# Kernel tuning notes

Hardware: AMD Instinct MI355X
Metric: run time of the kernel (lower is better)

## Reference

```python
import jax, jax.numpy as jnp
import numpy as np

B, N, C = 8, 4096, 512
H = 8
HD = C // H          # head_dim = 64
KS = 5               # dwc kernel size
FF = 3.0             # focusing factor


def setup_inputs() -> dict:
    key = jax.random.key(0)
    ks = jax.random.split(key, 8)
    s = 1.0 / np.sqrt(C)
    return {
        "x": jax.random.normal(ks[0], (B, N, C), dtype=jnp.float32),
        "Wq": jax.random.normal(ks[1], (C, C), dtype=jnp.float32) * s,
        "Wkv": jax.random.normal(ks[2], (C, 2 * C), dtype=jnp.float32) * s,
        "Wproj": jax.random.normal(ks[3], (C, C), dtype=jnp.float32) * s,
        "b_proj": jax.random.normal(ks[4], (C,), dtype=jnp.float32) * 0.01,
        "scale_param": jnp.zeros((1, 1, C), dtype=jnp.float32),  # nn.Parameter(zeros)
        "dwc_w": jax.random.normal(ks[5], (HD, 1, KS, KS), dtype=jnp.float32) * 0.1,
        "dwc_b": jax.random.normal(ks[6], (HD,), dtype=jnp.float32) * 0.01,
    }


def _focus(t):
    # power-focusing map: preserve L2 norm while sharpening via elementwise power
    n = jnp.linalg.norm(t, axis=-1, keepdims=True)
    tp = t ** FF
    return tp / jnp.linalg.norm(tp, axis=-1, keepdims=True) * n


def reference(x, Wq, Wkv, Wproj, b_proj, scale_param, dwc_w, dwc_b):
    b, n, cdim = x.shape
    q = jax.nn.relu(x @ Wq) + 1e-6                      # [B,N,C]
    kv = x @ Wkv
    k = jax.nn.relu(kv[..., :cdim]) + 1e-6              # [B,N,C]
    v = kv[..., cdim:]                                  # [B,N,C]
    scale = jax.nn.softplus(scale_param)
    q = _focus(q / scale)
    k = _focus(k / scale)

    def split_heads(t):  # b n (h c) -> (b h) n c
        return t.reshape(b, n, H, HD).transpose(0, 2, 1, 3).reshape(b * H, n, HD)

    q, k, v = split_heads(q), split_heads(k), split_heads(v)
    i = j = n; c = d = HD
    z = 1.0 / (jnp.einsum('bic,bc->bi', q, k.sum(axis=1)) + 1e-6)  # [(bh), n]
    if i * j * (c + d) > c * d * (i + j):
        # linear path: O(N*c*d)
        kvm = jnp.einsum('bjc,bjd->bcd', k, v)          # [(bh), c, d]
        out = jnp.einsum('bic,bcd,bi->bid', q, kvm, z)
    else:
        qk = jnp.einsum('bic,bjc->bij', q, k)
        out = jnp.einsum('bij,bjd,bi->bid', qk, v, z)

    num = int(n ** 0.5)  # 64; N must be a perfect square
    fm = q.reshape(b * H, num, num, HD).transpose(0, 3, 1, 2)  # b c w h
    fm = jax.lax.conv_general_dilated(
        fm, dwc_w, window_strides=(1, 1), padding='SAME',
        feature_group_count=HD,
        dimension_numbers=('NCHW', 'OIHW', 'NCHW')) + dwc_b[None, :, None, None]
    fm = fm.transpose(0, 2, 3, 1).reshape(b * H, n, HD)
    out = out + fm
    out = out.reshape(b, H, n, HD).transpose(0, 2, 1, 3).reshape(b, n, cdim)
    return out @ Wproj + b_proj
```

## Files before the change

kernel.cpp:

```cpp
#include <hip/hip_runtime.h>
#include <cstddef>
#include <cstdint>

#define B_ 8
#define N_ 4096
#define C_ 512
#define H_ 8
#define HD_ 64
#define BH_ 64

typedef short  bf16x8 __attribute__((ext_vector_type(8)));
typedef float  f32x4  __attribute__((ext_vector_type(4)));
typedef ushort u16x8  __attribute__((ext_vector_type(8)));
typedef ushort u16x4  __attribute__((ext_vector_type(4)));

__device__ __forceinline__ float softplusf(float p) {
  return (p > 20.f) ? p : log1pf(expf(p));
}

__device__ __forceinline__ ushort f2bf(float f) {
  union { float f; unsigned u; } c; c.f = f;
  const unsigned r = c.u + 0x7fffu + ((c.u >> 16) & 1u);
  return (ushort)(r >> 16);
}
__device__ __forceinline__ float bf2f(ushort h) {
  union { unsigned u; float f; } c; c.u = ((unsigned)h) << 16;
  return c.f;
}

#define GLOAD16(g, l)                                                        \
  __builtin_amdgcn_global_load_lds(                                          \
      (const __attribute__((address_space(1))) void*)(g),                    \
      (__attribute__((address_space(3))) void*)(l), 16, 0, 0)

__global__ void scale_kernel(const float* __restrict__ sp, float* __restrict__ sinv)
{
  const int c = threadIdx.x;
  sinv[c] = 1.f / softplusf(sp[c]);
}

__global__ __launch_bounds__(256) void cvt_hi(const float* __restrict__ in,
                                              ushort* __restrict__ hi)
{
  const size_t i = (size_t)blockIdx.x * 256 + threadIdx.x;
  const float4 a = ((const float4*)in)[i * 2];
  const float4 b = ((const float4*)in)[i * 2 + 1];
  const float f[8] = {a.x, a.y, a.z, a.w, b.x, b.y, b.z, b.w};
  u16x8 h;
  #pragma unroll
  for (int j = 0; j < 8; ++j) h[j] = f2bf(f[j]);
  *(u16x8*)&hi[i * 8] = h;
}

__global__ __launch_bounds__(256) void cvt_w_t(const float* __restrict__ in,
                                               ushort* __restrict__ hi, int Nn)
{
  const int t  = blockIdx.x * 256 + threadIdx.x;
  const int n  = t >> 6;
  const int k8 = (t & 63) * 8;
  u16x8 h;
  #pragma unroll
  for (int j = 0; j < 8; ++j) h[j] = f2bf(in[(size_t)(k8 + j) * Nn + n]);
  *(u16x8*)&hi[(size_t)n * 512 + k8] = h;
}

__global__ __launch_bounds__(512, 2) void gemm_bf16(
    const ushort* __restrict__ Ah, const ushort* __restrict__ Bh,
    const float* __restrict__ bias,
    ushort* __restrict__ ob0, ushort* __restrict__ ob1, ushort* __restrict__ ob2,
    float* __restrict__ outf,
    int ncolb, int s1, int s2, int r0, int r1, int r2)
{
  __shared__ ushort lds[2][32768];
  const int tid = threadIdx.x;
  const int bid = blockIdx.x;
  const int loc = bid >> 3;
  const int xcd = bid & 7;
  const int row0 = ((xcd << 4) + loc / ncolb) * 256;
  const int col0 = (loc % ncolb) * 256;

  const int lane = tid & 63;
  const int li   = lane & 15;
  const int kq   = lane >> 4;
  const int w    = tid >> 6;
  const int wr   = (w >> 2) * 128;
  const int wc   = (w & 3) * 64;
  const int wbase = tid & 448;

  f32x4 acc[8][4] = {};

  auto STAGE = [&](int buf, int t) {
    ushort* l = &lds[buf][0];
    const int k0 = t * 64;
    #pragma unroll
    for (int it = 0; it < 4; ++it) {
      const int c   = it * 512 + tid;
      const int cw  = it * 512 + wbase;
      const int kb  = c >> 8;
      const int row = c & 255;
      GLOAD16(Ah + (size_t)(row0 + row) * 512 + k0 + kb * 8, &l[cw * 8]);
    }
    #pragma unroll
    for (int it = 0; it < 4; ++it) {
      const int c   = it * 512 + tid;
      const int cw  = it * 512 + wbase;
      const int kb  = c >> 8;
      const int col = c & 255;
      GLOAD16(Bh + (size_t)(col0 + col) * 512 + k0 + kb * 8, &l[16384 + cw * 8]);
    }
  };

  auto COMPUTE = [&](int buf) {
    const ushort* l = &lds[buf][0];
    #pragma unroll
    for (int kk = 0; kk < 2; ++kk) {
      const int kb = kk * 4 + kq;
      bf16x8 bv[4];
      #pragma unroll
      for (int n = 0; n < 4; ++n)
        bv[n] = *(const bf16x8*)&l[16384 + (kb * 256 + wc + n * 16 + li) * 8];
      __builtin_amdgcn_s_setprio(1);
      #pragma unroll
      for (int m = 0; m < 8; ++m) {
        const bf16x8 av = *(const bf16x8*)&l[(kb * 256 + wr + m * 16 + li) * 8];
        #pragma unroll
        for (int n = 0; n < 4; ++n)
          acc[m][n] = __builtin_amdgcn_mfma_f32_16x16x32_bf16(av, bv[n], acc[m][n], 0, 0, 0);
      }
      __builtin_amdgcn_s_setprio(0);
    }
  };

  STAGE(0, 0);
  __syncthreads();
  #pragma unroll 1
  for (int t = 0; t < 3; ++t) {
    STAGE(1, 2 * t + 1);
    COMPUTE(0);
    __syncthreads();
    STAGE(0, 2 * t + 2);
    COMPUTE(1);
    __syncthreads();
  }
  STAGE(1, 7);
  COMPUTE(0);
  __syncthreads();
  COMPUTE(1);

  if (outf) {
    #pragma unroll
    for (int m = 0; m < 8; ++m)
      #pragma unroll
      for (int n = 0; n < 4; ++n) {
        const int col = col0 + wc + n * 16 + li;
        const int row = row0 + wr + m * 16 + kq * 4;
        const float bv = bias[col];
        #pragma unroll
        for (int r = 0; r < 4; ++r)
          outf[(size_t)(row + r) * 512 + col] = acc[m][n][r] + bv;
      }
  } else {
    ushort* dest; int cbase, relu;
    if (col0 < s1)      { dest = ob0; cbase = 0;  relu = r0; }
    else if (col0 < s2) { dest = ob1; cbase = s1; relu = r1; }
    else                { dest = ob2; cbase = s2; relu = r2; }
    #pragma unroll
    for (int m = 0; m < 8; ++m)
      #pragma unroll
      for (int n = 0; n < 4; ++n) {
        const int col = col0 + wc + n * 16 + li;
        const int row = row0 + wr + m * 16 + kq * 4;
        #pragma unroll
        for (int r = 0; r < 4; ++r) {
          float v = acc[m][n][r];
          if (relu) v = fmaxf(v, 0.f) + 1e-6f;
          dest[(size_t)(row + r) * 512 + (col - cbase)] = f2bf(v);
        }
      }
  }
}

__global__ __launch_bounds__(256) void focus2(ushort* __restrict__ qb, ushort* __restrict__ kb,
                                              const float* __restrict__ sinv)
{
  const int rid  = blockIdx.x * 4 + (threadIdx.x >> 6);
  const int lane = threadIdx.x & 63;
  ushort* t = (rid < B_ * N_) ? qb : kb;
  const int row = rid & (B_ * N_ - 1);
  ushort* p = t + (size_t)row * 512 + lane * 8;
  const u16x8 raw = *(const u16x8*)p;
  const float4 sa = *(const float4*)&sinv[lane * 8];
  const float4 sb = *(const float4*)&sinv[lane * 8 + 4];
  const float sc[8] = {sa.x, sa.y, sa.z, sa.w, sb.x, sb.y, sb.z, sb.w};
  float tv[8];
  float s2 = 0.f, s6 = 0.f;
  #pragma unroll
  for (int i = 0; i < 8; ++i) {
    const float x = bf2f(raw[i]) * sc[i];
    tv[i] = x;
    const float x3 = x * x * x;
    s2 = fmaf(x, x, s2);
    s6 = fmaf(x3, x3, s6);
  }
  #pragma unroll
  for (int off = 32; off > 0; off >>= 1) {
    s2 += __shfl_xor(s2, off);
    s6 += __shfl_xor(s6, off);
  }
  const float f = sqrtf(s2 / s6);
  u16x8 o;
  #pragma unroll
  for (int i = 0; i < 8; ++i) o[i] = f2bf(tv[i] * tv[i] * tv[i] * f);
  *(u16x8*)p = o;
}

__global__ __launch_bounds__(256) void kvm_kernel(
    const ushort* __restrict__ kf, const ushort* __restrict__ vf,
    float* __restrict__ kvmT, float* __restrict__ ksum)
{
  __shared__ float Ks[32][68];
  __shared__ float Vs[32][68];
  const int bh = blockIdx.x, bb = bh >> 3, h = bh & 7;
  const int n0 = blockIdx.y * 256;
  const int tid = threadIdx.x;
  const int tx = tid & 15, ty = tid >> 4;
  const int r  = tid >> 3;
  const int cg = (tid & 7) * 8;
  float acc[4][4] = {};
  float ks[8] = {};
  for (int nb = 0; nb < 256; nb += 32) {
    const size_t base = ((size_t)(bb * N_ + n0 + nb + r)) * 512 + h * 64 + cg;
    const u16x8 kraw = *(const u16x8*)&kf[base];
    const u16x8 vraw = *(const u16x8*)&vf[base];
    #pragma unroll
    for (int j = 0; j < 8; ++j) {
      const float kv = bf2f(kraw[j]);
      Ks[r][cg + j] = kv;
      ks[j] += kv;
      Vs[r][cg + j] = bf2f(vraw[j]);
    }
    __syncthreads();
    #pragma unroll
    for (int kk = 0; kk < 32; ++kk) {
      const float4 a = *(const float4*)&Ks[kk][ty * 4];
      const float4 c = *(const float4*)&Vs[kk][tx * 4];
      const float av[4] = {a.x, a.y, a.z, a.w};
      const float bv[4] = {c.x, c.y, c.z, c.w};
      #pragma unroll
      for (int i = 0; i < 4; ++i)
        #pragma unroll
        for (int j = 0; j < 4; ++j)
          acc[i][j] = fmaf(av[i], bv[j], acc[i][j]);
    }
    __syncthreads();
  }
  #pragma unroll
  for (int i = 0; i < 4; ++i)
    #pragma unroll
    for (int j = 0; j < 4; ++j)
      atomicAdd(&kvmT[(bh * 64 + tx * 4 + j) * 64 + ty * 4 + i], acc[i][j]);
  #pragma unroll
  for (int j = 0; j < 8; ++j) {
    float s = ks[j];
    s += __shfl_xor(s, 8);
    s += __shfl_xor(s, 16);
    s += __shfl_xor(s, 32);
    if ((tid & 56) == 0) atomicAdd(&ksum[bh * 64 + cg + j], s);
  }
}

__global__ __launch_bounds__(256, 3) void attnout_kernel(
    const ushort* __restrict__ qf, const float* __restrict__ kvmT,
    const float* __restrict__ ksum, ushort* __restrict__ out)
{
  __shared__ ushort As[8 * 256 * 8];
  __shared__ ushort Bs[8 * 64 * 8];
  __shared__ float zrow[256];
  __shared__ float ksl[64];
  const int bh = blockIdx.x, bb = bh >> 3, h = bh & 7;
  const int n0 = blockIdx.y * 256;
  const int tid = threadIdx.x;
  const int lane = tid & 63;
  const int li   = lane & 15;
  const int kq   = lane >> 4;
  const int wv   = tid >> 6;
  const int w64  = tid & 192;

  #pragma unroll
  for (int it = 0; it < 8; ++it) {
    const int c   = it * 256 + tid;
    const int cw  = it * 256 + w64;
    const int kb  = c >> 8;
    const int row = c & 255;
    GLOAD16(qf + ((size_t)(bb * N_ + n0 + row)) * 512 + h * 64 + kb * 8,
            &As[cw * 8]);
  }
  {
    const int d  = tid >> 2;
    const int cg = (tid & 3) * 16;
    const float* src = &kvmT[(size_t)(bh * 64 + d) * 64 + cg];
    const float4 f0 = *(const float4*)&src[0];
    const float4 f1 = *(const float4*)&src[4];
    const float4 f2 = *(const float4*)&src[8];
    const float4 f3 = *(const float4*)&src[12];
    u16x8 b0, b1;
    b0[0]=f2bf(f0.x); b0[1]=f2bf(f0.y); b0[2]=f2bf(f0.z); b0[3]=f2bf(f0.w);
    b0[4]=f2bf(f1.x); b0[5]=f2bf(f1.y); b0[6]=f2bf(f1.z); b0[7]=f2bf(f1.w);
    b1[0]=f2bf(f2.x); b1[1]=f2bf(f2.y); b1[2]=f2bf(f2.z); b1[3]=f2bf(f2.w);
    b1[4]=f2bf(f3.x); b1[5]=f2bf(f3.y); b1[6]=f2bf(f3.z); b1[7]=f2bf(f3.w);
    *(u16x8*)&Bs[(((cg >> 3)    ) * 64 + d) * 8] = b0;
    *(u16x8*)&Bs[(((cg >> 3) + 1) * 64 + d) * 8] = b1;
  }
  if (tid < 64) ksl[tid] = ksum[bh * 64 + tid];
  __syncthreads();

  {
    float p = 0.f;
    #pragma unroll
    for (int kb = 0; kb < 8; ++kb) {
      const u16x8 qv = *(const u16x8*)&As[(kb * 256 + tid) * 8];
      #pragma unroll
      for (int j = 0; j < 8; ++j) p = fmaf(bf2f(qv[j]), ksl[kb * 8 + j], p);
    }
    zrow[tid] = 1.f / (p + 1e-6f);
  }

  f32x4 acc[2][4][4];
  #pragma unroll
  for (int a = 0; a < 2; ++a)
    #pragma unroll
    for (int b = 0; b < 4; ++b)
      #pragma unroll
      for (int c = 0; c < 4; ++c) acc[a][b][c] = (f32x4){0.f, 0.f, 0.f, 0.f};
  #pragma unroll
  for (int kh = 0; kh < 2; ++kh) {
    bf16x8 bv[4];
    #pragma unroll
    for (int dt = 0; dt < 4; ++dt)
      bv[dt] = *(const bf16x8*)&Bs[((kh * 4 + kq) * 64 + dt * 16 + li) * 8];
    #pragma unroll
    for (int mt = 0; mt < 4; ++mt) {
      const bf16x8 av = *(const bf16x8*)&As[((kh * 4 + kq) * 256 + wv * 64 + mt * 16 + li) * 8];
      #pragma unroll
      for (int dt = 0; dt < 4; ++dt)
        acc[0][mt][dt] = __builtin_amdgcn_mfma_f32_16x16x32_bf16(av, bv[dt], acc[0][mt][dt], 0, 0, 0);
    }
  }
  __syncthreads();

  #pragma unroll
  for (int mt = 0; mt < 4; ++mt) {
    const float4 zv = *(const float4*)&zrow[wv * 64 + mt * 16 + kq * 4];
    const float za[4] = {zv.x, zv.y, zv.z, zv.w};
    const int rowb = n0 + wv * 64 + mt * 16 + kq * 4;
    #pragma unroll
    for (int dt = 0; dt < 4; ++dt) {
      const int col = h * 64 + dt * 16 + li;
      #pragma unroll
      for (int r = 0; r < 4; ++r)
        out[((size_t)(bb * N_ + rowb + r)) * 512 + col] = f2bf(acc[0][mt][dt][r] * za[r]);
    }
  }
}

__global__ __launch_bounds__(256) void dwconv_hi(
    const ushort* __restrict__ qf, const float* __restrict__ w,
    const float* __restrict__ wb, const ushort* __restrict__ ano,
    ushort* __restrict__ oh)
{
  __shared__ float ws_[64 * 25];
  const int tid = threadIdx.x;
  for (int i = tid; i < 64 * 25; i += 256) ws_[i] = w[i];
  __syncthreads();

  const int bh = blockIdx.x, bb = bh >> 3, h = bh & 7;
  const int hd = tid & 63;
  const int s  = blockIdx.y * 4 + (tid >> 6);
  const int x  = s & 63;
  const int y0 = (s >> 6) * 8;

  float wreg[25];
  #pragma unroll
  for (int i = 0; i < 25; ++i) wreg[i] = ws_[hd * 25 + i];

  float acc[8];
  const float bias = wb[hd];
  #pragma unroll
  for (int j = 0; j < 8; ++j) acc[j] = bias;

  const ushort* base = qf + (size_t)bb * N_ * 512 + h * 64 + hd;
  #pragma unroll
  for (int kx = 0; kx < 5; ++kx) {
    const int xx  = x + kx - 2;
    const bool xok = (unsigned)xx < 64u;
    const int xxc = min(max(xx, 0), 63);
    float col[12];
    #pragma unroll
    for (int r = 0; r < 12; ++r) {
      const int yy  = y0 + r - 2;
      const bool ok = xok && ((unsigned)yy < 64u);
      const int yyc = min(max(yy, 0), 63);
      const float v = bf2f(base[(size_t)(yyc * 64 + xxc) * 512]);
      col[r] = ok ? v : 0.f;
    }
    #pragma unroll
    for (int ky = 0; ky < 5; ++ky) {
      const float wv = wreg[ky * 5 + kx];
      #pragma unroll
      for (int j = 0; j < 8; ++j)
        acc[j] = fmaf(wv, col[j + ky], acc[j]);
    }
  }

  #pragma unroll
  for (int j = 0; j < 8; ++j) {
    const int p = (y0 + j) * 64 + x;
    const size_t idx = ((size_t)(bb * N_ + p)) * 512 + h * 64 + hd;
    oh[idx] = f2bf(bf2f(ano[idx]) + acc[j]);
  }
}

extern "C" void kernel_launch(void* const* d_in, const int* in_sizes, int n_in,
                              void* d_out, int out_size, void* d_ws, size_t ws_size,
                              hipStream_t stream) {
  (void)in_sizes; (void)n_in; (void)out_size; (void)ws_size;
  const float* x     = (const float*)d_in[0];
  const float* Wq    = (const float*)d_in[1];
  const float* Wkv   = (const float*)d_in[2];
  const float* Wp    = (const float*)d_in[3];
  const float* bp    = (const float*)d_in[4];
  const float* sp    = (const float*)d_in[5];
  const float* dwc_w = (const float*)d_in[6];
  const float* dwc_b = (const float*)d_in[7];
  float* out = (float*)d_out;

  char* ws = (char*)d_ws;
  ushort* xh   = (ushort*)ws;
  ushort* qbuf = (ushort*)(ws + 33554432ull);
  ushort* kbuf = (ushort*)(ws + 67108864ull);
  char*   w0   = ws + 100663296ull;
  ushort* Bqh  = (ushort*)w0;
  ushort* Bph  = Bqh + 786432;
  float*  kvmb = (float*)(Bph + 262144);
  float*  ksum = kvmb + 262144;
  float*  sinv = ksum + 4096;
  ushort* vbuf = (ushort*)d_out;
  ushort* ano  = kbuf;

  const int M = B_ * N_;

  scale_kernel<<<1, 512, 0, stream>>>(sp, sinv);
  cvt_hi<<<8192, 256, 0, stream>>>(x, xh);
  cvt_w_t<<<128, 256, 0, stream>>>(Wq, Bqh, 512);
  cvt_w_t<<<256, 256, 0, stream>>>(Wkv, Bqh + 262144, 1024);
  cvt_w_t<<<128, 256, 0, stream>>>(Wp, Bph, 512);
  gemm_bf16<<<768, 512, 0, stream>>>(
      xh, Bqh, nullptr, qbuf, kbuf, vbuf, nullptr, 6, 512, 1024, 1, 1, 0);
  focus2<<<2 * M / 4, 256, 0, stream>>>(qbuf, kbuf, sinv);
  hipMemsetAsync(kvmb, 0, (262144 + 4096) * sizeof(float), stream);
  kvm_kernel<<<dim3(BH_, 16), 256, 0, stream>>>(kbuf, vbuf, kvmb, ksum);
  attnout_kernel<<<dim3(BH_, N_ / 256), 256, 0, stream>>>(qbuf, kvmb, ksum, ano);
  dwconv_hi<<<dim3(BH_, 128), 256, 0, stream>>>(qbuf, dwc_w, dwc_b, ano, xh);
  gemm_bf16<<<256, 512, 0, stream>>>(
      xh, Bph, bp, nullptr, nullptr, nullptr, out, 2, 512, 512, 0, 0, 0);
}
```

Measured before the change: 318.3 us.

## Use bf16 MFMA in kvm kernel with swizzled LDS and register prefetch

```diff
diff --git a/kernel.cpp b/kernel.cpp
--- a/kernel.cpp
+++ b/kernel.cpp
@@ -214,58 +214,74 @@
   *(u16x8*)p = o;
 }
 
-__global__ __launch_bounds__(256) void kvm_kernel(
+__global__ __launch_bounds__(256, 2) void kvm_kernel(
     const ushort* __restrict__ kf, const ushort* __restrict__ vf,
     float* __restrict__ kvmT, float* __restrict__ ksum)
 {
-  __shared__ float Ks[32][68];
-  __shared__ float Vs[32][68];
+  __shared__ ushort KT[2048];
+  __shared__ ushort VT[2048];
   const int bh = blockIdx.x, bb = bh >> 3, h = bh & 7;
-  const int n0 = blockIdx.y * 256;
+  const int n0 = blockIdx.y * 512;
   const int tid = threadIdx.x;
-  const int tx = tid & 15, ty = tid >> 4;
-  const int r  = tid >> 3;
-  const int cg = (tid & 7) * 8;
-  float acc[4][4] = {};
+  const int lane = tid & 63;
+  const int li   = lane & 15;
+  const int kq   = lane >> 4;
+  const int w    = tid >> 6;
+  const int r    = tid >> 3;
+  const int cg   = (tid & 7) * 8;
+
+  f32x4 acc[4] = {};
   float ks[8] = {};
-  for (int nb = 0; nb < 256; nb += 32) {
-    const size_t base = ((size_t)(bb * N_ + n0 + nb + r)) * 512 + h * 64 + cg;
-    const u16x8 kraw = *(const u16x8*)&kf[base];
-    const u16x8 vraw = *(const u16x8*)&vf[base];
+
+  u16x8 kraw = *(const u16x8*)&kf[((size_t)(bb * N_ + n0 + r)) * 512 + h * 64 + cg];
+  u16x8 vraw = *(const u16x8*)&vf[((size_t)(bb * N_ + n0 + r)) * 512 + h * 64 + cg];
+
+  #pragma unroll 1
+  for (int t = 0; t < 16; ++t) {
+    u16x8 knext = kraw, vnext = vraw;
+    if (t < 15) {
+      const size_t gn = ((size_t)(bb * N_ + n0 + (t + 1) * 32 + r)) * 512 + h * 64 + cg;
+      knext = *(const u16x8*)&kf[gn];
+      vnext = *(const u16x8*)&vf[gn];
+    }
     #pragma unroll
     for (int j = 0; j < 8; ++j) {
-      const float kv = bf2f(kraw[j]);
-      Ks[r][cg + j] = kv;
-      ks[j] += kv;
-      Vs[r][cg + j] = bf2f(vraw[j]);
+      const int c = cg + j;
+      const int p = (r >> 3) ^ ((c ^ (c >> 3)) & 3);
+      const int idx = c * 32 + p * 8 + (r & 7);
+      KT[idx] = kraw[j];
+      VT[idx] = vraw[j];
+      ks[j] += bf2f(kraw[j]);
     }
     __syncthreads();
-    #pragma unroll
-    for (int kk = 0; kk < 32; ++kk) {
-      const float4 a = *(const float4*)&Ks[kk][ty * 4];
-      const float4 c = *(const float4*)&Vs[kk][tx * 4];
-      const float av[4] = {a.x, a.y, a.z, a.w};
-      const float bv[4] = {c.x, c.y, c.z, c.w};
-      #pragma unroll
-      for (int i = 0; i < 4; ++i)
-        #pragma unroll
-        for (int j = 0; j < 4; ++j)
-          acc[i][j] = fmaf(av[i], bv[j], acc[i][j]);
+    {
+      const int ca = w * 16 + li;
+      const bf16x8 av = *(const bf16x8*)&KT[ca * 32 + ((kq ^ ((ca ^ (ca >> 3)) & 3)) * 8)];
+      #pragma unroll
+      for (int dt = 0; dt < 4; ++dt) {
+        const int cb = dt * 16 + li;
+        const bf16x8 bv = *(const bf16x8*)&VT[cb * 32 + ((kq ^ ((cb ^ (cb >> 3)) & 3)) * 8)];
+        acc[dt] = __builtin_amdgcn_mfma_f32_16x16x32_bf16(av, bv, acc[dt], 0, 0, 0);
+      }
     }
     __syncthreads();
-  }
-  #pragma unroll
-  for (int i = 0; i < 4; ++i)
-    #pragma unroll
-    for (int j = 0; j < 4; ++j)
-      atomicAdd(&kvmT[(bh * 64 + tx * 4 + j) * 64 + ty * 4 + i], acc[i][j]);
+    kraw = knext;
+    vraw = vnext;
+  }
+
+  #pragma unroll
+  for (int dt = 0; dt < 4; ++dt)
+    #pragma unroll
+    for (int rr = 0; rr < 4; ++rr)
+      atomicAdd(&kvmT[(size_t)(bh * 64 + dt * 16 + li) * 64 + w * 16 + kq * 4 + rr],
+                acc[dt][rr]);
   #pragma unroll
   for (int j = 0; j < 8; ++j) {
     float s = ks[j];
     s += __shfl_xor(s, 8);
     s += __shfl_xor(s, 16);
     s += __shfl_xor(s, 32);
-    if ((tid & 56) == 0) atomicAdd(&ksum[bh * 64 + cg + j], s);
+    if ((lane & 56) == 0) atomicAdd(&ksum[bh * 64 + cg + j], s);
   }
 }
 
@@ -325,13 +341,7 @@
     zrow[tid] = 1.f / (p + 1e-6f);
   }
 
-  f32x4 acc[2][4][4];
-  #pragma unroll
-  for (int a = 0; a < 2; ++a)
-    #pragma unroll
-    for (int b = 0; b < 4; ++b)
-      #pragma unroll
-      for (int c = 0; c < 4; ++c) acc[a][b][c] = (f32x4){0.f, 0.f, 0.f, 0.f};
+  f32x4 acc[4] = {};
   #pragma unroll
   for (int kh = 0; kh < 2; ++kh) {
     bf16x8 bv[4];
@@ -341,9 +351,29 @@
     #pragma unroll
     for (int mt = 0; mt < 4; ++mt) {
       const bf16x8 av = *(const bf16x8*)&As[((kh * 4 + kq) * 256 + wv * 64 + mt * 16 + li) * 8];
+      acc[mt] = __builtin_amdgcn_mfma_f32_16x16x32_bf16(av, bv[0], acc[mt], 0, 0, 0);
+      (void)0;
+    }
+    #pragma unroll
+    for (int mt = 0; mt < 4; ++mt) {
+      const bf16x8 av = *(const bf16x8*)&As[((kh * 4 + kq) * 256 + wv * 64 + mt * 16 + li) * 8];
+      (void)av;
+    }
+    break;
+  }
+  f32x4 acc2[4][4] = {};
+  #pragma unroll
+  for (int kh = 0; kh < 2; ++kh) {
+    bf16x8 bv[4];
+    #pragma unroll
+    for (int dt = 0; dt < 4; ++dt)
+      bv[dt] = *(const bf16x8*)&Bs[((kh * 4 + kq) * 64 + dt * 16 + li) * 8];
+    #pragma unroll
+    for (int mt = 0; mt < 4; ++mt) {
+      const bf16x8 av = *(const bf16x8*)&As[((kh * 4 + kq) * 256 + wv * 64 + mt * 16 + li) * 8];
       #pragma unroll
       for (int dt = 0; dt < 4; ++dt)
-        acc[0][mt][dt] = __builtin_amdgcn_mfma_f32_16x16x32_bf16(av, bv[dt], acc[0][mt][dt], 0, 0, 0);
+        acc2[mt][dt] = __builtin_amdgcn_mfma_f32_16x16x32_bf16(av, bv[dt], acc2[mt][dt], 0, 0, 0);
     }
   }
   __syncthreads();
@@ -358,7 +388,7 @@
       const int col = h * 64 + dt * 16 + li;
       #pragma unroll
       for (int r = 0; r < 4; ++r)
-        out[((size_t)(bb * N_ + rowb + r)) * 512 + col] = f2bf(acc[0][mt][dt][r] * za[r]);
+        out[((size_t)(bb * N_ + rowb + r)) * 512 + col] = f2bf(acc2[mt][dt][r] * za[r]);
     }
   }
 }
@@ -458,7 +488,7 @@
       xh, Bqh, nullptr, qbuf, kbuf, vbuf, nullptr, 6, 512, 1024, 1, 1, 0);
   focus2<<<2 * M / 4, 256, 0, stream>>>(qbuf, kbuf, sinv);
   hipMemsetAsync(kvmb, 0, (262144 + 4096) * sizeof(float), stream);
-  kvm_kernel<<<dim3(BH_, 16), 256, 0, stream>>>(kbuf, vbuf, kvmb, ksum);
+  kvm_kernel<<<dim3(BH_, 8), 256, 0, stream>>>(kbuf, vbuf, kvmb, ksum);
   attnout_kernel<<<dim3(BH_, N_ / 256), 256, 0, stream>>>(qbuf, kvmb, ksum, ano);
   dwconv_hi<<<dim3(BH_, 128), 256, 0, stream>>>(qbuf, dwc_w, dwc_b, ano, xh);
   gemm_bf16<<<256, 512, 0, stream>>>(
```

New measurement: 286.4 us. 10.0% less time.
